# Optimization experiments

Hardware: AMD Instinct MI355X
Metric: run time of the kernel (lower is better)

## Reference

```python
import jax, jax.numpy as jnp
import numpy as np

B, S, D, E, K = 4, 4096, 2048, 64, 2


def setup_inputs() -> dict:
    key = jax.random.key(0)
    k1, k2 = jax.random.split(key)
    hidden_states = jax.random.normal(k1, (B, S, D), dtype=jnp.float32)
    gate_weight = jax.random.normal(k2, (E, D), dtype=jnp.float32) * 0.02
    return {"hidden_states": hidden_states, "gate_weight": gate_weight}


def reference(hidden_states, gate_weight):
    b, s, d = hidden_states.shape
    e = gate_weight.shape[0]
    n = b * s
    x = hidden_states.reshape(n, d)
    logits = x @ gate_weight.T                                  # [N, E]
    # Original reassigns gate_logits = softmax(gate_logits) in fp32.
    probs = jax.nn.softmax(logits.astype(jnp.float32), axis=-1)  # [N, E]

    top_v, top_i = jax.lax.top_k(probs, K)                       # [N, K]
    top_k_gates = top_v  # normalize_gate_prob_before_dropping=False

    oh = jax.nn.one_hot(top_i, e, dtype=probs.dtype)             # [N, K, E]
    gates = jnp.einsum('nke,nk->ne', oh, top_k_gates)            # scatter of top-k gates

    # Auxiliary losses (training path, use_aux_loss=True)
    gates_mean = gates.mean(axis=0)                              # [E]
    selection_mean = oh.sum(axis=(0, 1)) / n                     # [E]
    load_balancing_loss = (gates_mean * selection_mean).sum() * e
    # NOTE: original computes z-loss on the softmaxed probs (gate_logits was overwritten)
    router_z_loss = (jax.nn.logsumexp(probs, axis=-1) ** 2).mean()

    # torch scatter_ with index [B,S,1,1] only ever writes slot k=0.
    dispatch0 = oh.sum(axis=1).reshape(b, s, e)                  # 1.0 at top-k experts
    combine0 = gates.reshape(b, s, e)
    pad = ((0, 0), (0, 0), (0, 0), (0, K - 1))
    dispatch_tensor = jnp.pad(dispatch0[..., None], pad)         # [B,S,E,K]
    combine_tensor = jnp.pad(combine0[..., None], pad)           # [B,S,E,K]

    return dispatch_tensor, combine_tensor, load_balancing_loss, router_z_loss
```

## Files before the change

kernel.cpp:

```cpp
#include <hip/hip_runtime.h>
#include <hip/hip_bf16.h>
#include <cstddef>

namespace {
constexpr int kD = 2048;
constexpr int kE = 64;
constexpr int kN = 16384;
constexpr size_t kDispatchFloats = (size_t)kN * kE * 2;
constexpr size_t kWsplitOff = 1024;
}

typedef short short8_t __attribute__((ext_vector_type(8)));
typedef float f32x4 __attribute__((ext_vector_type(4)));

__device__ __forceinline__ void split3(float f, unsigned short& s1,
                                       unsigned short& s2, unsigned short& s3) {
  __hip_bfloat16 h1 = __float2bfloat16(f);
  float r1 = f - __bfloat162float(h1);
  __hip_bfloat16 h2 = __float2bfloat16(r1);
  float r2 = r1 - __bfloat162float(h2);
  __hip_bfloat16 h3 = __float2bfloat16(r2);
  s1 = __builtin_bit_cast(unsigned short, h1);
  s2 = __builtin_bit_cast(unsigned short, h2);
  s3 = __builtin_bit_cast(unsigned short, h3);
}

__device__ __forceinline__ void split8(f32x4 a, f32x4 b, short8_t& o1,
                                       short8_t& o2, short8_t& o3) {
  unsigned short s1, s2, s3;
#define SP(v, i, j) \
  split3((v)[i], s1, s2, s3); o1[j]=(short)s1; o2[j]=(short)s2; o3[j]=(short)s3;
  SP(a, 0, 0) SP(a, 1, 1) SP(a, 2, 2) SP(a, 3, 3)
  SP(b, 0, 4) SP(b, 1, 5) SP(b, 2, 6) SP(b, 3, 7)
#undef SP
}

__global__ __launch_bounds__(256)
void prep_kernel(const float* __restrict__ W, unsigned short* __restrict__ img,
                 float* __restrict__ ws) {
  const int t = blockIdx.x * 256 + threadIdx.x;
  if (t < 512) ws[t] = 0.0f;
  const int dq  = t >> 12;
  const int c   = (t >> 9) & 7;
  const int row = (t >> 3) & 63;
  const int cs8 = t & 7;
  const int co  = cs8 ^ (row & 7);
  const float* src = W + (size_t)row * kD + dq * 512 + c * 64 + co * 8;
  const float4 v0 = *reinterpret_cast<const float4*>(src);
  const float4 v1 = *reinterpret_cast<const float4*>(src + 4);
  short8_t o1, o2, o3;
  unsigned short s1, s2, s3;
  split3(v0.x, s1, s2, s3); o1[0]=(short)s1; o2[0]=(short)s2; o3[0]=(short)s3;
  split3(v0.y, s1, s2, s3); o1[1]=(short)s1; o2[1]=(short)s2; o3[1]=(short)s3;
  split3(v0.z, s1, s2, s3); o1[2]=(short)s1; o2[2]=(short)s2; o3[2]=(short)s3;
  split3(v0.w, s1, s2, s3); o1[3]=(short)s1; o2[3]=(short)s2; o3[3]=(short)s3;
  split3(v1.x, s1, s2, s3); o1[4]=(short)s1; o2[4]=(short)s2; o3[4]=(short)s3;
  split3(v1.y, s1, s2, s3); o1[5]=(short)s1; o2[5]=(short)s2; o3[5]=(short)s3;
  split3(v1.z, s1, s2, s3); o1[6]=(short)s1; o2[6]=(short)s2; o3[6]=(short)s3;
  split3(v1.w, s1, s2, s3); o1[7]=(short)s1; o2[7]=(short)s2; o3[7]=(short)s3;
  unsigned short* dst = img + (size_t)(dq * 8 + c) * 12288 + row * 64 + cs8 * 8;
  *reinterpret_cast<short8_t*>(dst + 0 * 4096) = o1;
  *reinterpret_cast<short8_t*>(dst + 1 * 4096) = o2;
  *reinterpret_cast<short8_t*>(dst + 2 * 4096) = o3;
}

__global__ __launch_bounds__(512, 4)
void logits_kernel(const float* __restrict__ x,
                   const unsigned short* __restrict__ wimg,
                   float* __restrict__ out) {
  __shared__ __attribute__((aligned(16))) unsigned char smem[40960];
  float* xsf = reinterpret_cast<float*>(smem);
  unsigned short (*wt)[64][64] =
      reinterpret_cast<unsigned short (*)[64][64]>(smem + 16384);

  const int tid  = threadIdx.x;
  const int lane = tid & 63;
  const int wv   = __builtin_amdgcn_readfirstlane(tid >> 6);
  const int wr   = wv >> 2;
  const int wc   = (wv >> 1) & 1;
  const int kh   = wv & 1;
  const int tile = blockIdx.x & 255;
  const int dq   = blockIdx.x >> 8;
  const int lrow = lane & 15;
  const int lk   = lane >> 4;

  const int row = tid >> 3, seg = tid & 7;
  const float4* __restrict__ bx = reinterpret_cast<const float4*>(x) +
      ((size_t)tile * 64 + row) * 512 + dq * 128 + seg * 2;
  const unsigned short* __restrict__ wbase =
      wimg + (size_t)dq * 8 * 12288 + tid * 8;
  unsigned short* wtf = &wt[0][0][0];
  const int sc0 = ((2 * seg) ^ (row & 15)) * 4;
  const int sc1 = ((2 * seg + 1) ^ (row & 15)) * 4;

  f32x4 acc[2][2];
  const f32x4 z4 = {0.0f, 0.0f, 0.0f, 0.0f};
  acc[0][0] = z4; acc[0][1] = z4; acc[1][0] = z4; acc[1][1] = z4;

  float4 vx0 = bx[0], vx1 = bx[1];

  for (int c = 0; c < 8; ++c) {
    const unsigned short* wsrc = wbase + (size_t)c * 12288;
#pragma unroll
    for (int i = 0; i < 3; ++i)
      __builtin_amdgcn_global_load_lds(
          (const __attribute__((address_space(1))) void*)(wsrc + i * 4096),
          (__attribute__((address_space(3))) void*)(wtf + i * 4096 + wv * 512),
          16, 0, 0);
    __builtin_amdgcn_sched_barrier(0);
    const float4 xa = vx0, xb = vx1;
    const int cn = (c + 1) & 7;
    vx0 = bx[cn * 16 + 0];
    vx1 = bx[cn * 16 + 1];
    *reinterpret_cast<float4*>(xsf + row * 64 + sc0) = xa;
    *reinterpret_cast<float4*>(xsf + row * 64 + sc1) = xb;
    asm volatile("s_waitcnt vmcnt(2) lgkmcnt(0)" ::: "memory");
    __builtin_amdgcn_sched_barrier(0);
    __builtin_amdgcn_s_barrier();
    __builtin_amdgcn_sched_barrier(0);
    __builtin_amdgcn_s_setprio(1);
    {
      const int kc = kh * 4 + lk;
      short8_t b1[2], b2[2], b3[2];
#pragma unroll
      for (int nt = 0; nt < 2; ++nt) {
        const int e = wc * 32 + nt * 16 + lrow;
        const int cw = (kc ^ (e & 7)) * 8;
        b1[nt] = *reinterpret_cast<const short8_t*>(&wt[0][e][cw]);
        b2[nt] = *reinterpret_cast<const short8_t*>(&wt[1][e][cw]);
        b3[nt] = *reinterpret_cast<const short8_t*>(&wt[2][e][cw]);
      }
#pragma unroll
      for (int mt = 0; mt < 2; ++mt) {
        const int ra = wr * 32 + mt * 16 + lrow;
        const int ca0 = ((2 * kc) ^ (ra & 15)) * 4;
        const int ca1 = ((2 * kc + 1) ^ (ra & 15)) * 4;
        const f32x4 va = *reinterpret_cast<const f32x4*>(xsf + ra * 64 + ca0);
        const f32x4 vb = *reinterpret_cast<const f32x4*>(xsf + ra * 64 + ca1);
        short8_t a1, a2, a3;
        split8(va, vb, a1, a2, a3);
#pragma unroll
        for (int nt = 0; nt < 2; ++nt) {
          acc[mt][nt] = __builtin_amdgcn_mfma_f32_16x16x32_bf16(a1, b1[nt], acc[mt][nt], 0, 0, 0);
          acc[mt][nt] = __builtin_amdgcn_mfma_f32_16x16x32_bf16(a1, b2[nt], acc[mt][nt], 0, 0, 0);
          acc[mt][nt] = __builtin_amdgcn_mfma_f32_16x16x32_bf16(a2, b1[nt], acc[mt][nt], 0, 0, 0);
          acc[mt][nt] = __builtin_amdgcn_mfma_f32_16x16x32_bf16(a1, b3[nt], acc[mt][nt], 0, 0, 0);
          acc[mt][nt] = __builtin_amdgcn_mfma_f32_16x16x32_bf16(a3, b1[nt], acc[mt][nt], 0, 0, 0);
          acc[mt][nt] = __builtin_amdgcn_mfma_f32_16x16x32_bf16(a2, b2[nt], acc[mt][nt], 0, 0, 0);
        }
      }
    }
    __builtin_amdgcn_s_setprio(0);
    __builtin_amdgcn_sched_barrier(0);
    __builtin_amdgcn_s_barrier();
  }

  float* __restrict__ mbuf = reinterpret_cast<float*>(smem + 16384);
  if (kh == 1) {
#pragma unroll
    for (int mt = 0; mt < 2; ++mt)
#pragma unroll
      for (int nt = 0; nt < 2; ++nt)
#pragma unroll
        for (int r = 0; r < 4; ++r) {
          const int trow = wr * 32 + mt * 16 + lk * 4 + r;
          const int col  = wc * 32 + nt * 16 + lrow;
          mbuf[trow * 65 + col] = acc[mt][nt][r];
        }
  }
  __syncthreads();
  if (kh == 0) {
    float* __restrict__ base = out + ((dq < 2) ? (size_t)0 : kDispatchFloats);
#pragma unroll
    for (int mt = 0; mt < 2; ++mt)
#pragma unroll
      for (int r = 0; r < 4; ++r) {
        const int trow = wr * 32 + mt * 16 + lk * 4 + r;
        const size_t n = (size_t)tile * 64 + trow;
        float* __restrict__ dst =
            base + n * 128 + (dq & 1) * 64 + wc * 32 + lrow;
#pragma unroll
        for (int nt = 0; nt < 2; ++nt) {
          const int col = wc * 32 + nt * 16 + lrow;
          dst[nt * 16] = acc[mt][nt][r] + mbuf[trow * 65 + col];
        }
      }
  }
}

__global__ __launch_bounds__(256)
void gate_kernel(float* __restrict__ out, float* __restrict__ ws) {
  __shared__ float lg[64][65];
  __shared__ int ti0[64], ti1[64];
  __shared__ float tv0[64], tv1[64], tz2[64];
  const int tid  = threadIdx.x;
  const int tile = blockIdx.x;

  float* __restrict__ outd = out + (size_t)tile * 8192;
  float* __restrict__ outc = out + kDispatchFloats + (size_t)tile * 8192;
  const float4* __restrict__ d4 = reinterpret_cast<const float4*>(outd);
  const float4* __restrict__ c4 = reinterpret_cast<const float4*>(outc);

  const int tq = tid >> 4, q = tid & 15;
#pragma unroll
  for (int k = 0; k < 4; ++k) {
    const int t = k * 16 + tq;
    const float4 a = d4[t * 32 + q];
    const float4 b = d4[t * 32 + 16 + q];
    const float4 c = c4[t * 32 + q];
    const float4 d = c4[t * 32 + 16 + q];
    lg[t][q * 4 + 0] = a.x + b.x + c.x + d.x;
    lg[t][q * 4 + 1] = a.y + b.y + c.y + d.y;
    lg[t][q * 4 + 2] = a.z + b.z + c.z + d.z;
    lg[t][q * 4 + 3] = a.w + b.w + c.w + d.w;
  }
  __syncthreads();

  if (tid < 64) {
    float v0 = -INFINITY, v1 = -INFINITY;
    int i0 = 0, i1 = 0;
    for (int e = 0; e < kE; ++e) {
      const float l = lg[tid][e];
      if (l > v0) { v1 = v0; i1 = i0; v0 = l; i0 = e; }
      else if (l > v1) { v1 = l; i1 = e; }
    }
    const float m = v0;
    float s = 0.0f;
    for (int e = 0; e < kE; ++e) s += __expf(lg[tid][e] - m);
    const float rs = 1.0f / s;
    float zexp = 0.0f;
    for (int e = 0; e < kE; ++e) zexp += __expf(__expf(lg[tid][e] - m) * rs);
    const float z = logf(zexp);
    ti0[tid] = i0; ti1[tid] = i1;
    tv0[tid] = rs;
    tv1[tid] = __expf(v1 - m) * rs;
    tz2[tid] = z * z;
  }
  __syncthreads();

  if (tid < kE) {
    float g = 0.0f, cnt = 0.0f;
    for (int t = 0; t < 64; ++t) {
      if (ti0[t] == tid) { g += tv0[t]; cnt += 1.0f; }
      if (ti1[t] == tid) { g += tv1[t]; cnt += 1.0f; }
    }
    atomicAdd(&ws[tid], g);
    atomicAdd(&ws[kE + tid], cnt);
    float z2 = tz2[tid];
    for (int off = 32; off; off >>= 1) z2 += __shfl_down(z2, off);
    if (tid == 0) atomicAdd(&ws[2 * kE], z2);
  }

  {
    const int t = tid >> 2, sub = tid & 3;
    const int i0 = ti0[t], i1 = ti1[t];
    const float v0 = tv0[t], v1 = tv1[t];
    float4* __restrict__ dp = reinterpret_cast<float4*>(outd) + t * 32;
    float4* __restrict__ cp = reinterpret_cast<float4*>(outc) + t * 32;
#pragma unroll
    for (int j = 0; j < 8; ++j) {
      const int qq = sub * 8 + j;
      const int e0 = qq * 2, e1 = qq * 2 + 1;
      const float d0v = (e0 == i0 || e0 == i1) ? 1.0f : 0.0f;
      const float d1v = (e1 == i0 || e1 == i1) ? 1.0f : 0.0f;
      const float c0 = (e0 == i0) ? v0 : ((e0 == i1) ? v1 : 0.0f);
      const float c1 = (e1 == i0) ? v0 : ((e1 == i1) ? v1 : 0.0f);
      dp[qq] = make_float4(d0v, 0.0f, d1v, 0.0f);
      cp[qq] = make_float4(c0, 0.0f, c1, 0.0f);
    }
  }
}

__global__ void finalize_kernel(const float* __restrict__ ws,
                                float* __restrict__ out) {
  const int e = threadIdx.x;
  float prod = ws[e] * ws[kE + e];
  for (int off = 32; off; off >>= 1) prod += __shfl_down(prod, off);
  if (e == 0) {
    const size_t base = kDispatchFloats * 2;
    const float invN = 1.0f / (float)kN;
    out[base]     = prod * ((float)kE * invN * invN);
    out[base + 1] = ws[2 * kE] * invN;
  }
}

extern "C" void kernel_launch(void* const* d_in, const int* in_sizes, int n_in,
                              void* d_out, int out_size, void* d_ws,
                              size_t ws_size, hipStream_t stream) {
  const float* x = (const float*)d_in[0];
  const float* W = (const float*)d_in[1];
  float* out = (float*)d_out;
  float* ws = (float*)d_ws;
  unsigned short* wimg = (unsigned short*)(ws + kWsplitOff);

  prep_kernel<<<64, 256, 0, stream>>>(W, wimg, ws);
  logits_kernel<<<1024, 512, 0, stream>>>(x, wimg, out);
  gate_kernel<<<256, 256, 0, stream>>>(out, ws);
  finalize_kernel<<<1, kE, 0, stream>>>(ws, out);
}
```

Before: 73.08 us.

## Fuse logits GEMM and gating into one kernel with full-K per block

The split-K logits kernel and the separate gate kernel are merged into one kernel. Each block now owns 32 tokens across the full hidden dimension, so partial logits are reduced in shared memory rather than written to the output buffer and read back. This removes a round trip of partial sums through global memory and one kernel launch. In exchange the grid shrinks to 512 blocks with 64KB of LDS each and occupancy hint 2, which lowers parallelism and latency hiding.

```diff
diff --git a/kernel.cpp b/kernel.cpp
--- a/kernel.cpp
+++ b/kernel.cpp
@@ -40,12 +40,11 @@
                  float* __restrict__ ws) {
   const int t = blockIdx.x * 256 + threadIdx.x;
   if (t < 512) ws[t] = 0.0f;
-  const int dq  = t >> 12;
-  const int c   = (t >> 9) & 7;
+  const int g   = t >> 9;
   const int row = (t >> 3) & 63;
   const int cs8 = t & 7;
   const int co  = cs8 ^ (row & 7);
-  const float* src = W + (size_t)row * kD + dq * 512 + c * 64 + co * 8;
+  const float* src = W + (size_t)row * kD + g * 64 + co * 8;
   const float4 v0 = *reinterpret_cast<const float4*>(src);
   const float4 v1 = *reinterpret_cast<const float4*>(src + 4);
   short8_t o1, o2, o3;
@@ -58,96 +57,96 @@
   split3(v1.y, s1, s2, s3); o1[5]=(short)s1; o2[5]=(short)s2; o3[5]=(short)s3;
   split3(v1.z, s1, s2, s3); o1[6]=(short)s1; o2[6]=(short)s2; o3[6]=(short)s3;
   split3(v1.w, s1, s2, s3); o1[7]=(short)s1; o2[7]=(short)s2; o3[7]=(short)s3;
-  unsigned short* dst = img + (size_t)(dq * 8 + c) * 12288 + row * 64 + cs8 * 8;
+  unsigned short* dst = img + (size_t)g * 12288 + row * 64 + cs8 * 8;
   *reinterpret_cast<short8_t*>(dst + 0 * 4096) = o1;
   *reinterpret_cast<short8_t*>(dst + 1 * 4096) = o2;
   *reinterpret_cast<short8_t*>(dst + 2 * 4096) = o3;
 }
 
-__global__ __launch_bounds__(512, 4)
-void logits_kernel(const float* __restrict__ x,
-                   const unsigned short* __restrict__ wimg,
-                   float* __restrict__ out) {
-  __shared__ __attribute__((aligned(16))) unsigned char smem[40960];
+__global__ __launch_bounds__(512, 2)
+void moe_kernel(const float* __restrict__ x,
+                const unsigned short* __restrict__ wimg,
+                float* __restrict__ out, float* __restrict__ ws) {
+  __shared__ __attribute__((aligned(16))) unsigned char smem[65536];
   float* xsf = reinterpret_cast<float*>(smem);
-  unsigned short (*wt)[64][64] =
-      reinterpret_cast<unsigned short (*)[64][64]>(smem + 16384);
+  unsigned short (*wt)[3][64][64] =
+      reinterpret_cast<unsigned short (*)[3][64][64]>(smem + 16384);
+  float (*lg)[65] = reinterpret_cast<float (*)[65]>(smem);
+  __shared__ int ti0[32], ti1[32];
+  __shared__ float tv0[32], tv1[32], tz2[32];
 
   const int tid  = threadIdx.x;
   const int lane = tid & 63;
   const int wv   = __builtin_amdgcn_readfirstlane(tid >> 6);
-  const int wr   = wv >> 2;
+  const int th   = wv >> 2;
   const int wc   = (wv >> 1) & 1;
   const int kh   = wv & 1;
-  const int tile = blockIdx.x & 255;
-  const int dq   = blockIdx.x >> 8;
+  const int tile = blockIdx.x;
   const int lrow = lane & 15;
   const int lk   = lane >> 4;
 
-  const int row = tid >> 3, seg = tid & 7;
+  const int row = tid >> 4, t16 = tid & 15;
   const float4* __restrict__ bx = reinterpret_cast<const float4*>(x) +
-      ((size_t)tile * 64 + row) * 512 + dq * 128 + seg * 2;
-  const unsigned short* __restrict__ wbase =
-      wimg + (size_t)dq * 8 * 12288 + tid * 8;
-  unsigned short* wtf = &wt[0][0][0];
-  const int sc0 = ((2 * seg) ^ (row & 15)) * 4;
-  const int sc1 = ((2 * seg + 1) ^ (row & 15)) * 4;
-
-  f32x4 acc[2][2];
+      ((size_t)tile * 32 + row) * 512 + t16 * 2;
+  const unsigned short* __restrict__ wbase = wimg + tid * 8;
+  unsigned short* wtf = &wt[0][0][0][0];
+  const int su0 = ((2 * t16) ^ (row & 31)) * 4;
+  const int su1 = ((2 * t16 + 1) ^ (row & 31)) * 4;
+
+  f32x4 acc[2];
   const f32x4 z4 = {0.0f, 0.0f, 0.0f, 0.0f};
-  acc[0][0] = z4; acc[0][1] = z4; acc[1][0] = z4; acc[1][1] = z4;
+  acc[0] = z4; acc[1] = z4;
 
   float4 vx0 = bx[0], vx1 = bx[1];
 
-  for (int c = 0; c < 8; ++c) {
-    const unsigned short* wsrc = wbase + (size_t)c * 12288;
-#pragma unroll
-    for (int i = 0; i < 3; ++i)
+  for (int c = 0; c < 16; ++c) {
+    const unsigned short* wsrc = wbase + (size_t)(2 * c) * 12288;
+#pragma unroll
+    for (int i = 0; i < 6; ++i)
       __builtin_amdgcn_global_load_lds(
           (const __attribute__((address_space(1))) void*)(wsrc + i * 4096),
           (__attribute__((address_space(3))) void*)(wtf + i * 4096 + wv * 512),
           16, 0, 0);
     __builtin_amdgcn_sched_barrier(0);
     const float4 xa = vx0, xb = vx1;
-    const int cn = (c + 1) & 7;
-    vx0 = bx[cn * 16 + 0];
-    vx1 = bx[cn * 16 + 1];
-    *reinterpret_cast<float4*>(xsf + row * 64 + sc0) = xa;
-    *reinterpret_cast<float4*>(xsf + row * 64 + sc1) = xb;
+    const int cn = (c + 1) & 15;
+    vx0 = bx[cn * 32 + 0];
+    vx1 = bx[cn * 32 + 1];
+    *reinterpret_cast<float4*>(xsf + row * 128 + su0) = xa;
+    *reinterpret_cast<float4*>(xsf + row * 128 + su1) = xb;
     asm volatile("s_waitcnt vmcnt(2) lgkmcnt(0)" ::: "memory");
     __builtin_amdgcn_sched_barrier(0);
     __builtin_amdgcn_s_barrier();
     __builtin_amdgcn_sched_barrier(0);
     __builtin_amdgcn_s_setprio(1);
-    {
-      const int kc = kh * 4 + lk;
+#pragma unroll
+    for (int ks = 0; ks < 2; ++ks) {
+      const int kc = ks * 4 + lk;
       short8_t b1[2], b2[2], b3[2];
 #pragma unroll
       for (int nt = 0; nt < 2; ++nt) {
         const int e = wc * 32 + nt * 16 + lrow;
         const int cw = (kc ^ (e & 7)) * 8;
-        b1[nt] = *reinterpret_cast<const short8_t*>(&wt[0][e][cw]);
-        b2[nt] = *reinterpret_cast<const short8_t*>(&wt[1][e][cw]);
-        b3[nt] = *reinterpret_cast<const short8_t*>(&wt[2][e][cw]);
+        b1[nt] = *reinterpret_cast<const short8_t*>(&wt[kh][0][e][cw]);
+        b2[nt] = *reinterpret_cast<const short8_t*>(&wt[kh][1][e][cw]);
+        b3[nt] = *reinterpret_cast<const short8_t*>(&wt[kh][2][e][cw]);
       }
-#pragma unroll
-      for (int mt = 0; mt < 2; ++mt) {
-        const int ra = wr * 32 + mt * 16 + lrow;
-        const int ca0 = ((2 * kc) ^ (ra & 15)) * 4;
-        const int ca1 = ((2 * kc + 1) ^ (ra & 15)) * 4;
-        const f32x4 va = *reinterpret_cast<const f32x4*>(xsf + ra * 64 + ca0);
-        const f32x4 vb = *reinterpret_cast<const f32x4*>(xsf + ra * 64 + ca1);
-        short8_t a1, a2, a3;
-        split8(va, vb, a1, a2, a3);
-#pragma unroll
-        for (int nt = 0; nt < 2; ++nt) {
-          acc[mt][nt] = __builtin_amdgcn_mfma_f32_16x16x32_bf16(a1, b1[nt], acc[mt][nt], 0, 0, 0);
-          acc[mt][nt] = __builtin_amdgcn_mfma_f32_16x16x32_bf16(a1, b2[nt], acc[mt][nt], 0, 0, 0);
-          acc[mt][nt] = __builtin_amdgcn_mfma_f32_16x16x32_bf16(a2, b1[nt], acc[mt][nt], 0, 0, 0);
-          acc[mt][nt] = __builtin_amdgcn_mfma_f32_16x16x32_bf16(a1, b3[nt], acc[mt][nt], 0, 0, 0);
-          acc[mt][nt] = __builtin_amdgcn_mfma_f32_16x16x32_bf16(a3, b1[nt], acc[mt][nt], 0, 0, 0);
-          acc[mt][nt] = __builtin_amdgcn_mfma_f32_16x16x32_bf16(a2, b2[nt], acc[mt][nt], 0, 0, 0);
-        }
+      const int ra = th * 16 + lrow;
+      const int u0 = kh * 16 + ks * 8 + 2 * lk;
+      const int ca0 = ((u0) ^ (ra & 31)) * 4;
+      const int ca1 = ((u0 + 1) ^ (ra & 31)) * 4;
+      const f32x4 va = *reinterpret_cast<const f32x4*>(xsf + ra * 128 + ca0);
+      const f32x4 vb = *reinterpret_cast<const f32x4*>(xsf + ra * 128 + ca1);
+      short8_t a1, a2, a3;
+      split8(va, vb, a1, a2, a3);
+#pragma unroll
+      for (int nt = 0; nt < 2; ++nt) {
+        acc[nt] = __builtin_amdgcn_mfma_f32_16x16x32_bf16(a1, b1[nt], acc[nt], 0, 0, 0);
+        acc[nt] = __builtin_amdgcn_mfma_f32_16x16x32_bf16(a1, b2[nt], acc[nt], 0, 0, 0);
+        acc[nt] = __builtin_amdgcn_mfma_f32_16x16x32_bf16(a2, b1[nt], acc[nt], 0, 0, 0);
+        acc[nt] = __builtin_amdgcn_mfma_f32_16x16x32_bf16(a1, b3[nt], acc[nt], 0, 0, 0);
+        acc[nt] = __builtin_amdgcn_mfma_f32_16x16x32_bf16(a3, b1[nt], acc[nt], 0, 0, 0);
+        acc[nt] = __builtin_amdgcn_mfma_f32_16x16x32_bf16(a2, b2[nt], acc[nt], 0, 0, 0);
       }
     }
     __builtin_amdgcn_s_setprio(0);
@@ -155,68 +154,27 @@
     __builtin_amdgcn_s_barrier();
   }
 
-  float* __restrict__ mbuf = reinterpret_cast<float*>(smem + 16384);
   if (kh == 1) {
 #pragma unroll
-    for (int mt = 0; mt < 2; ++mt)
-#pragma unroll
-      for (int nt = 0; nt < 2; ++nt)
-#pragma unroll
-        for (int r = 0; r < 4; ++r) {
-          const int trow = wr * 32 + mt * 16 + lk * 4 + r;
-          const int col  = wc * 32 + nt * 16 + lrow;
-          mbuf[trow * 65 + col] = acc[mt][nt][r];
-        }
+    for (int nt = 0; nt < 2; ++nt)
+#pragma unroll
+      for (int r = 0; r < 4; ++r)
+        lg[th * 16 + lk * 4 + r][wc * 32 + nt * 16 + lrow] = acc[nt][r];
   }
   __syncthreads();
   if (kh == 0) {
-    float* __restrict__ base = out + ((dq < 2) ? (size_t)0 : kDispatchFloats);
-#pragma unroll
-    for (int mt = 0; mt < 2; ++mt)
+#pragma unroll
+    for (int nt = 0; nt < 2; ++nt)
 #pragma unroll
       for (int r = 0; r < 4; ++r) {
-        const int trow = wr * 32 + mt * 16 + lk * 4 + r;
-        const size_t n = (size_t)tile * 64 + trow;
-        float* __restrict__ dst =
-            base + n * 128 + (dq & 1) * 64 + wc * 32 + lrow;
-#pragma unroll
-        for (int nt = 0; nt < 2; ++nt) {
-          const int col = wc * 32 + nt * 16 + lrow;
-          dst[nt * 16] = acc[mt][nt][r] + mbuf[trow * 65 + col];
-        }
+        const int t = th * 16 + lk * 4 + r;
+        const int e = wc * 32 + nt * 16 + lrow;
+        lg[t][e] += acc[nt][r];
       }
   }
-}
-
-__global__ __launch_bounds__(256)
-void gate_kernel(float* __restrict__ out, float* __restrict__ ws) {
-  __shared__ float lg[64][65];
-  __shared__ int ti0[64], ti1[64];
-  __shared__ float tv0[64], tv1[64], tz2[64];
-  const int tid  = threadIdx.x;
-  const int tile = blockIdx.x;
-
-  float* __restrict__ outd = out + (size_t)tile * 8192;
-  float* __restrict__ outc = out + kDispatchFloats + (size_t)tile * 8192;
-  const float4* __restrict__ d4 = reinterpret_cast<const float4*>(outd);
-  const float4* __restrict__ c4 = reinterpret_cast<const float4*>(outc);
-
-  const int tq = tid >> 4, q = tid & 15;
-#pragma unroll
-  for (int k = 0; k < 4; ++k) {
-    const int t = k * 16 + tq;
-    const float4 a = d4[t * 32 + q];
-    const float4 b = d4[t * 32 + 16 + q];
-    const float4 c = c4[t * 32 + q];
-    const float4 d = c4[t * 32 + 16 + q];
-    lg[t][q * 4 + 0] = a.x + b.x + c.x + d.x;
-    lg[t][q * 4 + 1] = a.y + b.y + c.y + d.y;
-    lg[t][q * 4 + 2] = a.z + b.z + c.z + d.z;
-    lg[t][q * 4 + 3] = a.w + b.w + c.w + d.w;
-  }
   __syncthreads();
 
-  if (tid < 64) {
+  if (tid < 32) {
     float v0 = -INFINITY, v1 = -INFINITY;
     int i0 = 0, i1 = 0;
     for (int e = 0; e < kE; ++e) {
@@ -240,26 +198,34 @@
 
   if (tid < kE) {
     float g = 0.0f, cnt = 0.0f;
-    for (int t = 0; t < 64; ++t) {
+    for (int t = 0; t < 32; ++t) {
       if (ti0[t] == tid) { g += tv0[t]; cnt += 1.0f; }
       if (ti1[t] == tid) { g += tv1[t]; cnt += 1.0f; }
     }
     atomicAdd(&ws[tid], g);
     atomicAdd(&ws[kE + tid], cnt);
+  }
+  if (tid < 32) {
     float z2 = tz2[tid];
-    for (int off = 32; off; off >>= 1) z2 += __shfl_down(z2, off);
+    z2 += __shfl_down(z2, 16);
+    z2 += __shfl_down(z2, 8);
+    z2 += __shfl_down(z2, 4);
+    z2 += __shfl_down(z2, 2);
+    z2 += __shfl_down(z2, 1);
     if (tid == 0) atomicAdd(&ws[2 * kE], z2);
   }
 
   {
-    const int t = tid >> 2, sub = tid & 3;
+    const int t = tid >> 4, sub = tid & 15;
     const int i0 = ti0[t], i1 = ti1[t];
     const float v0 = tv0[t], v1 = tv1[t];
-    float4* __restrict__ dp = reinterpret_cast<float4*>(outd) + t * 32;
-    float4* __restrict__ cp = reinterpret_cast<float4*>(outc) + t * 32;
-#pragma unroll
-    for (int j = 0; j < 8; ++j) {
-      const int qq = sub * 8 + j;
+    const size_t n = (size_t)tile * 32 + t;
+    float4* __restrict__ dp = reinterpret_cast<float4*>(out) + n * 32;
+    float4* __restrict__ cp =
+        reinterpret_cast<float4*>(out) + kDispatchFloats / 4 + n * 32;
+#pragma unroll
+    for (int j = 0; j < 2; ++j) {
+      const int qq = sub * 2 + j;
       const int e0 = qq * 2, e1 = qq * 2 + 1;
       const float d0v = (e0 == i0 || e0 == i1) ? 1.0f : 0.0f;
       const float d1v = (e1 == i0 || e1 == i1) ? 1.0f : 0.0f;
@@ -294,7 +260,6 @@
   unsigned short* wimg = (unsigned short*)(ws + kWsplitOff);
 
   prep_kernel<<<64, 256, 0, stream>>>(W, wimg, ws);
-  logits_kernel<<<1024, 512, 0, stream>>>(x, wimg, out);
-  gate_kernel<<<256, 256, 0, stream>>>(out, ws);
+  moe_kernel<<<512, 512, 0, stream>>>(x, wimg, out, ws);
   finalize_kernel<<<1, kE, 0, stream>>>(ws, out);
 }
```

Result: faster. 69.29 us (-5.2%).
